# Kernel optimization log

Hardware: AMD Instinct MI355X
Metric: run time of the kernel (lower is better)

## Reference

```python
import jax, jax.numpy as jnp
import numpy as np

N = 16384      # num_nodes
E = 524288     # num_edges (avg degree 32)
B = 32         # batch_size
D = 64         # input_dim
OUT = 64       # output_dim
K = 2          # max_diffusion_step
M = 2 * K + 1  # num_matrices = len(supports)*K + 1


def setup_inputs() -> dict:
    key = jax.random.key(0)
    k1, k2, k3, k4, k5 = jax.random.split(key, 5)
    inputs = jax.random.normal(k1, (B, N, D), dtype=jnp.float32)
    rows = jax.random.randint(k2, (E,), 0, N)
    cols = jax.random.randint(k3, (E,), 0, N)
    adj_vals = jax.random.uniform(k4, (E,), dtype=jnp.float32)
    # xavier_normal_ init for weights [D*M, OUT]
    std = (2.0 / (D * M + OUT)) ** 0.5
    weights = jax.random.normal(k5, (D * M, OUT), dtype=jnp.float32) * std
    biases = jnp.zeros((1, OUT), dtype=jnp.float32)  # bias_start = 0.0
    return dict(inputs=inputs, adj_vals=adj_vals, rows=rows, cols=cols,
                weights=weights, biases=biases)


def _spmm(vals, src, dst, x):
    # y[dst] += vals * x[src]; x: [N, F]  (sparse matrix-vector over edge list)
    return jax.ops.segment_sum(vals[:, None] * x[src], dst, num_segments=N)


def reference(inputs, adj_vals, rows, cols, weights, biases):
    b, n, d = inputs.shape
    # calculate_random_walk_matrix(A) = D_row^{-1} A ; support1 = its transpose
    # calculate_random_walk_matrix(A^T) = D_col^{-1} A^T ; support2 = its transpose
    drow = jax.ops.segment_sum(adj_vals, rows, num_segments=N)
    dcol = jax.ops.segment_sum(adj_vals, cols, num_segments=N)
    inv_drow = jnp.where(drow > 0, 1.0 / drow, 0.0)
    inv_dcol = jnp.where(dcol > 0, 1.0 / dcol, 0.0)
    vals1 = adj_vals * inv_drow[rows]  # support1 @ x: gather src=rows, scatter dst=cols
    vals2 = adj_vals * inv_dcol[cols]  # support2 @ x: gather src=cols, scatter dst=rows
    supports = [(vals1, rows, cols), (vals2, cols, rows)]

    # x0 layout: permute(1,2,0) -> [N, D, B] -> [N, D*B]
    x0 = jnp.transpose(inputs, (1, 2, 0)).reshape(n, d * b)
    xs = [x0]
    for vals, src, dst in supports:
        x1 = _spmm(vals, src, dst, x0)
        xs.append(x1)
        for _ in range(2, K + 1):
            x2 = 2.0 * _spmm(vals, src, dst, x1) - x0
            xs.append(x2)
            x1, x0 = x2, x1  # NOTE: x0 deliberately NOT reset between supports (matches torch src)
    x = jnp.stack(xs, axis=0).reshape(M, n, d, b)       # [M, N, D, B]
    x = jnp.transpose(x, (3, 1, 2, 0)).reshape(b * n, d * M)  # [B*N, D*M]
    out = x @ weights + biases
    return out.reshape(b, n, OUT)
```

## Files before the change

### kernel.cpp

```cpp
#include <hip/hip_runtime.h>
#include <stdint.h>

#define NN 16384
#define EE 524288
#define BB 32
#define DD 64
#define OO 64
#define MM 5
#define KK 320

typedef __attribute__((ext_vector_type(2))) _Float16 half2_t;
typedef __attribute__((ext_vector_type(8))) _Float16 half8_t;
typedef __attribute__((ext_vector_type(4))) float floatx4;

__global__ __launch_bounds__(256) void hist_kernel(
    const float* __restrict__ adj, const int* __restrict__ rows,
    const int* __restrict__ cols,
    float* __restrict__ drow, float* __restrict__ dcol,
    int* __restrict__ cnt_row, int* __restrict__ cnt_col)
{
    int e = blockIdx.x * 256 + threadIdx.x;
    if (e < EE) {
        float a = adj[e];
        int r = rows[e], c = cols[e];
        atomicAdd(&drow[r], a);
        atomicAdd(&dcol[c], a);
        atomicAdd(&cnt_row[r], 1);
        atomicAdd(&cnt_col[c], 1);
    }
}

__global__ __launch_bounds__(1024) void scan_kernel(
    const int* __restrict__ cnt_col, const int* __restrict__ cnt_row,
    int* __restrict__ off_col, int* __restrict__ off_row,
    int* __restrict__ cur_col, int* __restrict__ cur_row)
{
    const int* cnt = (blockIdx.x == 0) ? cnt_col : cnt_row;
    int* off = (blockIdx.x == 0) ? off_col : off_row;
    int* cur = (blockIdx.x == 0) ? cur_col : cur_row;

    __shared__ int part[1024];
    int t = threadIdx.x;
    int base = t * 16;
    int local[16];
    int s = 0;
#pragma unroll
    for (int i = 0; i < 16; i++) { local[i] = cnt[base + i]; s += local[i]; }
    part[t] = s;
    __syncthreads();
    for (int d = 1; d < 1024; d <<= 1) {
        int v = (t >= d) ? part[t - d] : 0;
        __syncthreads();
        part[t] += v;
        __syncthreads();
    }
    int run = (t == 0) ? 0 : part[t - 1];
#pragma unroll
    for (int i = 0; i < 16; i++) {
        off[base + i] = run;
        cur[base + i] = run;
        run += local[i];
    }
    if (t == 1023) off[NN] = run;
}

__global__ __launch_bounds__(256) void scatter_kernel(
    const float* __restrict__ adj, const int* __restrict__ rows,
    const int* __restrict__ cols,
    const float* __restrict__ drow, const float* __restrict__ dcol,
    int* __restrict__ cur_col, int* __restrict__ cur_row,
    int2* __restrict__ edge1, int2* __restrict__ edge2)
{
    int e = blockIdx.x * 256 + threadIdx.x;
    if (e < EE) {
        float a = adj[e];
        int r = rows[e], c = cols[e];
        float dr = drow[r];
        float idr = (dr > 0.f) ? (1.f / dr) : 0.f;
        float dc = dcol[c];
        float idc = (dc > 0.f) ? (1.f / dc) : 0.f;
        _Float16 h1 = (_Float16)(a * idr);
        _Float16 h2 = (_Float16)(a * idc);
        unsigned short u1 = __builtin_bit_cast(unsigned short, h1);
        unsigned short u2 = __builtin_bit_cast(unsigned short, h2);
        int p1 = atomicAdd(&cur_col[c], 1);
        edge1[p1] = make_int2(r, (int)(u1 | ((unsigned int)u1 << 16)));
        int p2 = atomicAdd(&cur_row[r], 1);
        edge2[p2] = make_int2(c, (int)(u2 | ((unsigned int)u2 << 16)));
    }
}

__global__ __launch_bounds__(256) void cast_kernel(
    const float* __restrict__ inp, unsigned short* __restrict__ x0)
{
    size_t i = ((size_t)blockIdx.x * 256 + threadIdx.x) * 8;
    float4 a = *(const float4*)(inp + i);
    float4 b = *(const float4*)(inp + i + 4);
    half2_t h0 = {(_Float16)a.x, (_Float16)a.y};
    half2_t h1 = {(_Float16)a.z, (_Float16)a.w};
    half2_t h2 = {(_Float16)b.x, (_Float16)b.y};
    half2_t h3 = {(_Float16)b.z, (_Float16)b.w};
    uint4 o;
    o.x = __builtin_bit_cast(unsigned int, h0);
    o.y = __builtin_bit_cast(unsigned int, h1);
    o.z = __builtin_bit_cast(unsigned int, h2);
    o.w = __builtin_bit_cast(unsigned int, h3);
    *(uint4*)(x0 + i) = o;
}

__global__ __launch_bounds__(256) void wprep_kernel(
    const float* __restrict__ W, unsigned short* __restrict__ Wt)
{
    int i = blockIdx.x * 256 + threadIdx.x;
    if (i < OO * KK) {
        int o = i / KK;
        int kp = i - o * KK;
        int m = kp >> 6;
        int d = kp & 63;
        _Float16 h = (_Float16)W[(d * MM + m) * OO + o];
        Wt[i] = __builtin_bit_cast(unsigned short, h);
    }
}

__global__ __launch_bounds__(256) void spmm_kernel(
    const unsigned short* __restrict__ xin,
    const unsigned short* __restrict__ z,
    unsigned short* __restrict__ xout,
    const int* __restrict__ off, const int2* __restrict__ edges,
    float alpha, float beta, int has_z)
{
    unsigned int l = blockIdx.x;
    int xcd  = l & 7;
    unsigned int s = l >> 3;
    int bhi  = s >> 9;
    int ntile = s & 511;
    int b = bhi * 8 + xcd;

    int t = threadIdx.x;
    int n = ntile * 32 + (t >> 3);
    unsigned int dgb = (unsigned int)(t & 7) * 16u;
    int e0 = off[n], e1 = off[n + 1];
    const char* xbB = (const char*)(xin + (size_t)b * NN * DD);

    half2_t acc0 = (half2_t)0, acc1 = (half2_t)0, acc2 = (half2_t)0, acc3 = (half2_t)0;

#define FMA4(V, W2)                                                       \
    do {                                                                  \
        acc0 = __builtin_bit_cast(half2_t, (V).x) * (W2) + acc0;          \
        acc1 = __builtin_bit_cast(half2_t, (V).y) * (W2) + acc1;          \
        acc2 = __builtin_bit_cast(half2_t, (V).z) * (W2) + acc2;          \
        acc3 = __builtin_bit_cast(half2_t, (V).w) * (W2) + acc3;          \
    } while (0)

    int ecnt = e1 - e0;
    int nb4 = ecnt >> 2;

    int2 ed0, ed1, ed2, ed3;
    if (nb4 > 0) {
        ed0 = edges[e0];
        ed1 = edges[e0 + 1];
        ed2 = edges[e0 + 2];
        ed3 = edges[e0 + 3];
    }
    for (int it = 0; it < nb4; ++it) {
        uint4 v0 = *(const uint4*)(xbB + (((unsigned int)ed0.x) << 7) + dgb);
        uint4 v1 = *(const uint4*)(xbB + (((unsigned int)ed1.x) << 7) + dgb);
        uint4 v2 = *(const uint4*)(xbB + (((unsigned int)ed2.x) << 7) + dgb);
        uint4 v3 = *(const uint4*)(xbB + (((unsigned int)ed3.x) << 7) + dgb);
        half2_t w0 = __builtin_bit_cast(half2_t, ed0.y);
        half2_t w1 = __builtin_bit_cast(half2_t, ed1.y);
        half2_t w2 = __builtin_bit_cast(half2_t, ed2.y);
        half2_t w3 = __builtin_bit_cast(half2_t, ed3.y);

        int2 nd0, nd1, nd2, nd3;
        int enext = e0 + (it + 1) * 4;
        if (it + 1 < nb4) {
            nd0 = edges[enext];
            nd1 = edges[enext + 1];
            nd2 = edges[enext + 2];
            nd3 = edges[enext + 3];
        }

        FMA4(v0, w0);
        FMA4(v1, w1);
        FMA4(v2, w2);
        FMA4(v3, w3);

        ed0 = nd0; ed1 = nd1; ed2 = nd2; ed3 = nd3;
    }
    for (int e = e0 + nb4 * 4; e < e1; ++e) {
        int2 ed = edges[e];
        half2_t wv = __builtin_bit_cast(half2_t, ed.y);
        uint4 v = *(const uint4*)(xbB + (((unsigned int)ed.x) << 7) + dgb);
        FMA4(v, wv);
    }
#undef FMA4

    size_t fo = ((size_t)b * NN + n) * DD + (dgb >> 1);
    if (has_z) {
        uint4 zv = *(const uint4*)(z + fo);
        half2_t al = {(_Float16)alpha, (_Float16)alpha};
        half2_t be = {(_Float16)beta, (_Float16)beta};
        acc0 = al * acc0 + be * __builtin_bit_cast(half2_t, zv.x);
        acc1 = al * acc1 + be * __builtin_bit_cast(half2_t, zv.y);
        acc2 = al * acc2 + be * __builtin_bit_cast(half2_t, zv.z);
        acc3 = al * acc3 + be * __builtin_bit_cast(half2_t, zv.w);
    }

    uint4 o;
    o.x = __builtin_bit_cast(unsigned int, acc0);
    o.y = __builtin_bit_cast(unsigned int, acc1);
    o.z = __builtin_bit_cast(unsigned int, acc2);
    o.w = __builtin_bit_cast(unsigned int, acc3);
    *(uint4*)(xout + fo) = o;
}

__global__ __launch_bounds__(256, 4) void final_mfma(
    const unsigned short* __restrict__ X0, const unsigned short* __restrict__ X1,
    const unsigned short* __restrict__ X2, const unsigned short* __restrict__ X3,
    const unsigned short* __restrict__ X4,
    const unsigned short* __restrict__ Wt, const float* __restrict__ bias,
    float* __restrict__ out)
{
    int blk = blockIdx.x;
    int b = blk >> 6;
    int n0 = (blk & 63) * 256;
    int t = threadIdx.x;
    int wave = t >> 6;
    int lane = t & 63;
    int col = lane & 15;
    int quad = lane >> 4;

    size_t rowbase = (size_t)b * NN + n0 + wave * 64;

    floatx4 acc[4][4];
#pragma unroll
    for (int ct = 0; ct < 4; ct++)
#pragma unroll
        for (int rt = 0; rt < 4; rt++) acc[ct][rt] = (floatx4){0.f, 0.f, 0.f, 0.f};

#define KSTEP(XP, m, h)                                                          \
    {                                                                            \
        const unsigned short* xa = (XP) + rowbase * DD + (h) * 32 + quad * 8;    \
        half8_t a0 = *(const half8_t*)(xa + (0 * 16 + col) * DD);                \
        half8_t a1 = *(const half8_t*)(xa + (1 * 16 + col) * DD);                \
        half8_t a2 = *(const half8_t*)(xa + (2 * 16 + col) * DD);                \
        half8_t a3 = *(const half8_t*)(xa + (3 * 16 + col) * DD);                \
        const unsigned short* wb = Wt + ((m) * 2 + (h)) * 32 + quad * 8;         \
        half8_t b0 = *(const half8_t*)(wb + (0 * 16 + col) * KK);                \
        half8_t b1 = *(const half8_t*)(wb + (1 * 16 + col) * KK);                \
        half8_t b2 = *(const half8_t*)(wb + (2 * 16 + col) * KK);                \
        half8_t b3 = *(const half8_t*)(wb + (3 * 16 + col) * KK);                \
        acc[0][0] = __builtin_amdgcn_mfma_f32_16x16x32_f16(a0, b0, acc[0][0], 0, 0, 0); \
        acc[0][1] = __builtin_amdgcn_mfma_f32_16x16x32_f16(a1, b0, acc[0][1], 0, 0, 0); \
        acc[0][2] = __builtin_amdgcn_mfma_f32_16x16x32_f16(a2, b0, acc[0][2], 0, 0, 0); \
        acc[0][3] = __builtin_amdgcn_mfma_f32_16x16x32_f16(a3, b0, acc[0][3], 0, 0, 0); \
        acc[1][0] = __builtin_amdgcn_mfma_f32_16x16x32_f16(a0, b1, acc[1][0], 0, 0, 0); \
        acc[1][1] = __builtin_amdgcn_mfma_f32_16x16x32_f16(a1, b1, acc[1][1], 0, 0, 0); \
        acc[1][2] = __builtin_amdgcn_mfma_f32_16x16x32_f16(a2, b1, acc[1][2], 0, 0, 0); \
        acc[1][3] = __builtin_amdgcn_mfma_f32_16x16x32_f16(a3, b1, acc[1][3], 0, 0, 0); \
        acc[2][0] = __builtin_amdgcn_mfma_f32_16x16x32_f16(a0, b2, acc[2][0], 0, 0, 0); \
        acc[2][1] = __builtin_amdgcn_mfma_f32_16x16x32_f16(a1, b2, acc[2][1], 0, 0, 0); \
        acc[2][2] = __builtin_amdgcn_mfma_f32_16x16x32_f16(a2, b2, acc[2][2], 0, 0, 0); \
        acc[2][3] = __builtin_amdgcn_mfma_f32_16x16x32_f16(a3, b2, acc[2][3], 0, 0, 0); \
        acc[3][0] = __builtin_amdgcn_mfma_f32_16x16x32_f16(a0, b3, acc[3][0], 0, 0, 0); \
        acc[3][1] = __builtin_amdgcn_mfma_f32_16x16x32_f16(a1, b3, acc[3][1], 0, 0, 0); \
        acc[3][2] = __builtin_amdgcn_mfma_f32_16x16x32_f16(a2, b3, acc[3][2], 0, 0, 0); \
        acc[3][3] = __builtin_amdgcn_mfma_f32_16x16x32_f16(a3, b3, acc[3][3], 0, 0, 0); \
    }

    KSTEP(X0, 0, 0)
    KSTEP(X0, 0, 1)
    KSTEP(X1, 1, 0)
    KSTEP(X1, 1, 1)
    KSTEP(X2, 2, 0)
    KSTEP(X2, 2, 1)
    KSTEP(X3, 3, 0)
    KSTEP(X3, 3, 1)
    KSTEP(X4, 4, 0)
    KSTEP(X4, 4, 1)
#undef KSTEP

#pragma unroll
    for (int ct = 0; ct < 4; ct++) {
        int o = ct * 16 + col;
        float bv = bias[o];
#pragma unroll
        for (int rt = 0; rt < 4; rt++) {
            size_t rb = rowbase + rt * 16 + quad * 4;
#pragma unroll
            for (int r = 0; r < 4; r++) {
                out[(rb + r) * OO + o] = acc[ct][rt][r] + bv;
            }
        }
    }
}

extern "C" void kernel_launch(void* const* d_in, const int* in_sizes, int n_in,
                              void* d_out, int out_size, void* d_ws, size_t ws_size,
                              hipStream_t stream)
{
    (void)in_sizes; (void)n_in; (void)out_size; (void)ws_size;
    const float* inputs  = (const float*)d_in[0];
    const float* adj     = (const float*)d_in[1];
    const int*   rows    = (const int*)d_in[2];
    const int*   cols    = (const int*)d_in[3];
    const float* weights = (const float*)d_in[4];
    const float* bias    = (const float*)d_in[5];
    float* out = (float*)d_out;

    char* ws = (char*)d_ws;
    size_t off = 0;
    auto alloc = [&](size_t bytes) -> char* {
        char* p = ws + off;
        off = (off + bytes + 255) & ~(size_t)255;
        return p;
    };
    float* drow    = (float*)alloc(NN * 4);
    float* dcol    = (float*)alloc(NN * 4);
    int* cnt_col   = (int*)alloc(NN * 4);
    int* cnt_row   = (int*)alloc(NN * 4);
    int* off_col   = (int*)alloc((NN + 1) * 4);
    int* off_row   = (int*)alloc((NN + 1) * 4);
    int* cur_col   = (int*)alloc(NN * 4);
    int* cur_row   = (int*)alloc(NN * 4);
    int2* edge1    = (int2*)alloc((size_t)EE * 8);
    int2* edge2    = (int2*)alloc((size_t)EE * 8);
    unsigned short* Wt = (unsigned short*)alloc((size_t)OO * KK * 2);
    unsigned short* X[MM];
    for (int m = 0; m < MM; m++) X[m] = (unsigned short*)alloc((size_t)NN * BB * DD * 2);

    hipMemsetAsync(drow, 0, (size_t)NN * 4 * 4, stream);

    hist_kernel<<<EE / 256, 256, 0, stream>>>(adj, rows, cols, drow, dcol,
                                              cnt_row, cnt_col);
    scan_kernel<<<2, 1024, 0, stream>>>(cnt_col, cnt_row, off_col, off_row,
                                        cur_col, cur_row);
    scatter_kernel<<<EE / 256, 256, 0, stream>>>(adj, rows, cols, drow, dcol,
                                                 cur_col, cur_row, edge1, edge2);
    cast_kernel<<<(BB * NN * DD) / (256 * 8), 256, 0, stream>>>(inputs, X[0]);
    wprep_kernel<<<(OO * KK + 255) / 256, 256, 0, stream>>>(weights, Wt);

    const int SPMM_GRID = 512 * BB;

    spmm_kernel<<<SPMM_GRID, 256, 0, stream>>>(X[0], nullptr, X[1], off_col,
                                               edge1, 1.f, 0.f, 0);
    spmm_kernel<<<SPMM_GRID, 256, 0, stream>>>(X[1], X[0], X[2], off_col,
                                               edge1, 2.f, -1.f, 1);
    spmm_kernel<<<SPMM_GRID, 256, 0, stream>>>(X[1], nullptr, X[3], off_row,
                                               edge2, 1.f, 0.f, 0);
    spmm_kernel<<<SPMM_GRID, 256, 0, stream>>>(X[3], X[1], X[4], off_row,
                                               edge2, 2.f, -1.f, 1);

    final_mfma<<<BB * (NN / 256), 256, 0, stream>>>(X[0], X[1], X[2], X[3], X[4],
                                                    Wt, bias, out);
}
```

Baseline: 1.039 ms.

## Sort nodes by degree for SpMM load balance and unroll edge loop by eight

Adds a counting-sort kernel that orders nodes by their in-degree, so each SpMM block processes nodes of similar degree. This reduces intra-wave divergence from the uneven edge counts. The SpMM inner loop is also unrolled from 4 to 8 gathers per iteration, with unconditional prefetch of the next edge batch, to get more memory-level parallelism. The cost is an extra small kernel, an indirection load per thread, scattered output writes and more register pressure.

```diff
diff --git a/kernel.cpp b/kernel.cpp
--- a/kernel.cpp
+++ b/kernel.cpp
@@ -62,6 +62,40 @@
         run += local[i];
     }
     if (t == 1023) off[NN] = run;
+}
+
+__global__ __launch_bounds__(1024) void degsort_kernel(
+    const int* __restrict__ off_col, const int* __restrict__ off_row,
+    int* __restrict__ perm_col, int* __restrict__ perm_row)
+{
+    const int* off = (blockIdx.x == 0) ? off_col : off_row;
+    int* perm = (blockIdx.x == 0) ? perm_col : perm_row;
+
+    __shared__ int bins[512];
+    __shared__ int cur[512];
+    int t = threadIdx.x;
+    if (t < 512) bins[t] = 0;
+    __syncthreads();
+    for (int i = t; i < NN; i += 1024) {
+        int d = off[i + 1] - off[i];
+        if (d > 511) d = 511;
+        atomicAdd(&bins[d], 1);
+    }
+    __syncthreads();
+    for (int sh = 1; sh < 512; sh <<= 1) {
+        int v = (t < 512 && t >= sh) ? bins[t - sh] : 0;
+        __syncthreads();
+        if (t < 512) bins[t] += v;
+        __syncthreads();
+    }
+    if (t < 512) cur[t] = (t == 0) ? 0 : bins[t - 1];
+    __syncthreads();
+    for (int i = t; i < NN; i += 1024) {
+        int d = off[i + 1] - off[i];
+        if (d > 511) d = 511;
+        int p = atomicAdd(&cur[d], 1);
+        perm[p] = i;
+    }
 }
 
 __global__ __launch_bounds__(256) void scatter_kernel(
@@ -126,7 +160,8 @@
     const unsigned short* __restrict__ xin,
     const unsigned short* __restrict__ z,
     unsigned short* __restrict__ xout,
-    const int* __restrict__ off, const int2* __restrict__ edges,
+    const int* __restrict__ off, const int* __restrict__ perm,
+    const int2* __restrict__ edges,
     float alpha, float beta, int has_z)
 {
     unsigned int l = blockIdx.x;
@@ -137,13 +172,14 @@
     int b = bhi * 8 + xcd;
 
     int t = threadIdx.x;
-    int n = ntile * 32 + (t >> 3);
+    int n = perm[ntile * 32 + (t >> 3)];
     unsigned int dgb = (unsigned int)(t & 7) * 16u;
     int e0 = off[n], e1 = off[n + 1];
     const char* xbB = (const char*)(xin + (size_t)b * NN * DD);
 
     half2_t acc0 = (half2_t)0, acc1 = (half2_t)0, acc2 = (half2_t)0, acc3 = (half2_t)0;
 
+#define GATHER(ED) (*(const uint4*)(xbB + (((unsigned int)(ED).x) << 7) + dgb))
 #define FMA4(V, W2)                                                       \
     do {                                                                  \
         acc0 = __builtin_bit_cast(half2_t, (V).x) * (W2) + acc0;          \
@@ -153,48 +189,59 @@
     } while (0)
 
     int ecnt = e1 - e0;
-    int nb4 = ecnt >> 2;
-
-    int2 ed0, ed1, ed2, ed3;
-    if (nb4 > 0) {
-        ed0 = edges[e0];
-        ed1 = edges[e0 + 1];
-        ed2 = edges[e0 + 2];
-        ed3 = edges[e0 + 3];
-    }
-    for (int it = 0; it < nb4; ++it) {
-        uint4 v0 = *(const uint4*)(xbB + (((unsigned int)ed0.x) << 7) + dgb);
-        uint4 v1 = *(const uint4*)(xbB + (((unsigned int)ed1.x) << 7) + dgb);
-        uint4 v2 = *(const uint4*)(xbB + (((unsigned int)ed2.x) << 7) + dgb);
-        uint4 v3 = *(const uint4*)(xbB + (((unsigned int)ed3.x) << 7) + dgb);
+    int nb8 = ecnt >> 3;
+
+    int2 ed0, ed1, ed2, ed3, ed4, ed5, ed6, ed7;
+    if (nb8 > 0) {
+        ed0 = edges[e0];     ed1 = edges[e0 + 1];
+        ed2 = edges[e0 + 2]; ed3 = edges[e0 + 3];
+        ed4 = edges[e0 + 4]; ed5 = edges[e0 + 5];
+        ed6 = edges[e0 + 6]; ed7 = edges[e0 + 7];
+    }
+    for (int it = 0; it < nb8; ++it) {
+        uint4 v0 = GATHER(ed0);
+        uint4 v1 = GATHER(ed1);
+        uint4 v2 = GATHER(ed2);
+        uint4 v3 = GATHER(ed3);
+        uint4 v4 = GATHER(ed4);
+        uint4 v5 = GATHER(ed5);
+        uint4 v6 = GATHER(ed6);
+        uint4 v7 = GATHER(ed7);
         half2_t w0 = __builtin_bit_cast(half2_t, ed0.y);
         half2_t w1 = __builtin_bit_cast(half2_t, ed1.y);
         half2_t w2 = __builtin_bit_cast(half2_t, ed2.y);
         half2_t w3 = __builtin_bit_cast(half2_t, ed3.y);
-
-        int2 nd0, nd1, nd2, nd3;
-        int enext = e0 + (it + 1) * 4;
-        if (it + 1 < nb4) {
-            nd0 = edges[enext];
-            nd1 = edges[enext + 1];
-            nd2 = edges[enext + 2];
-            nd3 = edges[enext + 3];
-        }
+        half2_t w4 = __builtin_bit_cast(half2_t, ed4.y);
+        half2_t w5 = __builtin_bit_cast(half2_t, ed5.y);
+        half2_t w6 = __builtin_bit_cast(half2_t, ed6.y);
+        half2_t w7 = __builtin_bit_cast(half2_t, ed7.y);
+
+        int ep = (it + 1 < nb8) ? (e0 + (it + 1) * 8) : e0;
+        int2 nd0 = edges[ep];     int2 nd1 = edges[ep + 1];
+        int2 nd2 = edges[ep + 2]; int2 nd3 = edges[ep + 3];
+        int2 nd4 = edges[ep + 4]; int2 nd5 = edges[ep + 5];
+        int2 nd6 = edges[ep + 6]; int2 nd7 = edges[ep + 7];
 
         FMA4(v0, w0);
         FMA4(v1, w1);
         FMA4(v2, w2);
         FMA4(v3, w3);
+        FMA4(v4, w4);
+        FMA4(v5, w5);
+        FMA4(v6, w6);
+        FMA4(v7, w7);
 
         ed0 = nd0; ed1 = nd1; ed2 = nd2; ed3 = nd3;
-    }
-    for (int e = e0 + nb4 * 4; e < e1; ++e) {
+        ed4 = nd4; ed5 = nd5; ed6 = nd6; ed7 = nd7;
+    }
+    for (int e = e0 + nb8 * 8; e < e1; ++e) {
         int2 ed = edges[e];
         half2_t wv = __builtin_bit_cast(half2_t, ed.y);
-        uint4 v = *(const uint4*)(xbB + (((unsigned int)ed.x) << 7) + dgb);
+        uint4 v = GATHER(ed);
         FMA4(v, wv);
     }
 #undef FMA4
+#undef GATHER
 
     size_t fo = ((size_t)b * NN + n) * DD + (dgb >> 1);
     if (has_z) {
@@ -324,6 +371,8 @@
     int* off_row   = (int*)alloc((NN + 1) * 4);
     int* cur_col   = (int*)alloc(NN * 4);
     int* cur_row   = (int*)alloc(NN * 4);
+    int* perm_col  = (int*)alloc(NN * 4);
+    int* perm_row  = (int*)alloc(NN * 4);
     int2* edge1    = (int2*)alloc((size_t)EE * 8);
     int2* edge2    = (int2*)alloc((size_t)EE * 8);
     unsigned short* Wt = (unsigned short*)alloc((size_t)OO * KK * 2);
@@ -336,6 +385,7 @@
                                               cnt_row, cnt_col);
     scan_kernel<<<2, 1024, 0, stream>>>(cnt_col, cnt_row, off_col, off_row,
                                         cur_col, cur_row);
+    degsort_kernel<<<2, 1024, 0, stream>>>(off_col, off_row, perm_col, perm_row);
     scatter_kernel<<<EE / 256, 256, 0, stream>>>(adj, rows, cols, drow, dcol,
                                                  cur_col, cur_row, edge1, edge2);
     cast_kernel<<<(BB * NN * DD) / (256 * 8), 256, 0, stream>>>(inputs, X[0]);
@@ -344,13 +394,13 @@
     const int SPMM_GRID = 512 * BB;
 
     spmm_kernel<<<SPMM_GRID, 256, 0, stream>>>(X[0], nullptr, X[1], off_col,
-                                               edge1, 1.f, 0.f, 0);
+                                               perm_col, edge1, 1.f, 0.f, 0);
     spmm_kernel<<<SPMM_GRID, 256, 0, stream>>>(X[1], X[0], X[2], off_col,
-                                               edge1, 2.f, -1.f, 1);
+                                               perm_col, edge1, 2.f, -1.f, 1);
     spmm_kernel<<<SPMM_GRID, 256, 0, stream>>>(X[1], nullptr, X[3], off_row,
-                                               edge2, 1.f, 0.f, 0);
+                                               perm_row, edge2, 1.f, 0.f, 0);
     spmm_kernel<<<SPMM_GRID, 256, 0, stream>>>(X[3], X[1], X[4], off_row,
-                                               edge2, 2.f, -1.f, 1);
+                                               perm_row, edge2, 2.f, -1.f, 1);
 
     final_mfma<<<BB * (NN / 256), 256, 0, stream>>>(X[0], X[1], X[2], X[3], X[4],
                                                     Wt, bias, out);
```

New measurement: 1.025 ms. No clear change (-1.3%).
